# Performance work log

Hardware: AMD Instinct MI355X
Metric: run time of the kernel (lower is better)

The kernel has to match this reference:

```python
import jax, jax.numpy as jnp
import numpy as np

B, S, D, DFF, E, TOP_K = 4, 2048, 1024, 4096, 8, 2


def setup_inputs() -> dict:
    key = jax.random.key(0)
    ks = jax.random.split(key, 6)
    s = 0.02
    return {
        "x": jax.random.normal(ks[0], (B, S, D), dtype=jnp.float32),
        "gate_w": jax.random.normal(ks[1], (E, D), dtype=jnp.float32) * s,
        "w1": jax.random.normal(ks[2], (E, DFF, D), dtype=jnp.float32) * s,
        "b1": jax.random.normal(ks[3], (E, DFF), dtype=jnp.float32) * s,
        "w2": jax.random.normal(ks[4], (E, D, DFF), dtype=jnp.float32) * s,
        "b2": jax.random.normal(ks[5], (E, D), dtype=jnp.float32) * s,
    }


def _moe_forward(x, gate_w, w1, b1, w2, b2):
    b, s, d = x.shape
    xf = x.reshape(-1, d)                      # [T, D]
    T = xf.shape[0]
    e = gate_w.shape[0]
    logits = xf @ gate_w.T                     # [T, E]
    top_v, top_i = jax.lax.top_k(logits, TOP_K)  # [T, K]
    gw = jax.nn.softmax(top_v, axis=-1)          # [T, K]
    # load-balance loss (Switch Transformers): E * sum_i f_i * P_i
    probs = jax.nn.softmax(logits, axis=-1)
    f = jnp.mean(jax.nn.one_hot(jnp.argmax(logits, axis=-1), e, dtype=x.dtype), axis=0)
    lb_loss = e * jnp.sum(f * probs.mean(axis=0))
    # dense per-expert FFN (exact GELU, matching torch F.gelu default)
    h = jax.nn.gelu(jnp.einsum('td,efd->tef', xf, w1) + b1, approximate=False)  # [T,E,DFF]
    eo = jnp.einsum('tef,edf->ted', h, w2) + b2                                  # [T,E,D]
    # scatter top-k gate weights into dense [T, E] combine weights
    cw = jnp.zeros((T, e), dtype=x.dtype).at[jnp.arange(T)[:, None], top_i].add(gw)
    out = jnp.einsum('te,ted->td', cw, eo).reshape(b, s, d)
    return out, lb_loss


def reference(x, gate_w, w1, b1, w2, b2):
    return _moe_forward(x, gate_w, w1, b1, w2, b2)
```

## Files before the change

kernel.cpp:

```cpp
#include <hip/hip_runtime.h>
#include <cstdint>
#include <cstddef>

#define NEXP 8
#define NTOK 8192
#define DMODEL 1024
#define DFFN 4096
#define CAP 17408

typedef __bf16 bf16;
typedef bf16 bf16x8 __attribute__((ext_vector_type(8)));
typedef float f32x4 __attribute__((ext_vector_type(4)));

static constexpr size_t OFF_HDR  = 0;
static constexpr size_t OFF_CNTH = 4096;
static constexpr size_t OFF_AMH  = OFF_CNTH + 65536;
static constexpr size_t OFF_PSH  = OFF_AMH + 65536;
static constexpr size_t OFF_TOKE = OFF_PSH + 65536;
static constexpr size_t OFF_TOKG = OFF_TOKE + 65536;
static constexpr size_t OFF_TOKS = OFF_TOKG + 65536;
static constexpr size_t OFF_BB   = OFF_TOKS + 65536;
static constexpr size_t OFF_XG   = OFF_BB + 65536;
static constexpr size_t OFF_W1B  = OFF_XG  + (size_t)CAP * DMODEL * 2;
static constexpr size_t OFF_W2B  = OFF_W1B + (size_t)NEXP * DFFN * DMODEL * 2;
static constexpr size_t OFF_H    = OFF_W2B + (size_t)NEXP * DMODEL * DFFN * 2;
static constexpr size_t OFF_O    = OFF_H   + (size_t)CAP * DFFN * 2;


__global__ void k_zero16(uint4* __restrict__ p) {
    p[(size_t)blockIdx.x * 256 + threadIdx.x] = make_uint4(0u, 0u, 0u, 0u);
}

__global__ void k_cvt(const float* __restrict__ s, bf16* __restrict__ d, int n8) {
    int i = blockIdx.x * 256 + threadIdx.x;
    if (i >= n8) return;
    const float4* sp = (const float4*)s;
    float4 a = sp[2 * i], b = sp[2 * i + 1];
    bf16x8 pk;
    pk[0] = (bf16)a.x; pk[1] = (bf16)a.y; pk[2] = (bf16)a.z; pk[3] = (bf16)a.w;
    pk[4] = (bf16)b.x; pk[5] = (bf16)b.y; pk[6] = (bf16)b.z; pk[7] = (bf16)b.w;
    ((bf16x8*)d)[i] = pk;
}

__global__ void k_gate(const float* __restrict__ x, const float* __restrict__ gwt,
                       int* __restrict__ cnth, int* __restrict__ amh, float* __restrict__ psh,
                       int* __restrict__ toke, float* __restrict__ tokg) {
    int tid = threadIdx.x, w = tid >> 6, lane = tid & 63;
    int t = blockIdx.x * 4 + w;
    __shared__ int s_cnt[8]; __shared__ int s_am[8]; __shared__ float s_ps[8];
    if (tid < 8) { s_cnt[tid] = 0; s_am[tid] = 0; s_ps[tid] = 0.f; }
    __syncthreads();
    float acc[8] = {0.f,0.f,0.f,0.f,0.f,0.f,0.f,0.f};
    const float4* xr = (const float4*)(x + (size_t)t * DMODEL);
#pragma unroll
    for (int c = 0; c < 4; c++) {
        float4 xv = xr[c * 64 + lane];
#pragma unroll
        for (int e = 0; e < 8; e++) {
            float4 wv = ((const float4*)(gwt + e * DMODEL))[c * 64 + lane];
            acc[e] = fmaf(xv.x, wv.x, fmaf(xv.y, wv.y, fmaf(xv.z, wv.z, fmaf(xv.w, wv.w, acc[e]))));
        }
    }
#pragma unroll
    for (int o = 32; o; o >>= 1) {
#pragma unroll
        for (int e = 0; e < 8; e++) acc[e] += __shfl_xor(acc[e], o);
    }
    if (lane == 0) {
        int i0 = 0; float v0 = acc[0];
#pragma unroll
        for (int e = 1; e < 8; e++) if (acc[e] > v0) { v0 = acc[e]; i0 = e; }
        int i1 = -1; float v1 = -1e30f;
#pragma unroll
        for (int e = 0; e < 8; e++) if (e != i0 && acc[e] > v1) { v1 = acc[e]; i1 = e; }
        float ex = expf(v1 - v0);
        float g0 = 1.f / (1.f + ex);
        float g1 = ex / (1.f + ex);
        toke[2 * t] = i0; toke[2 * t + 1] = i1;
        tokg[2 * t] = g0; tokg[2 * t + 1] = g1;
        atomicAdd(&s_cnt[i0], 1); atomicAdd(&s_cnt[i1], 1); atomicAdd(&s_am[i0], 1);
        float p[8], sum = 0.f;
#pragma unroll
        for (int e = 0; e < 8; e++) { p[e] = expf(acc[e] - v0); sum += p[e]; }
        float inv = 1.f / sum;
#pragma unroll
        for (int e = 0; e < 8; e++) atomicAdd(&s_ps[e], p[e] * inv);
    }
    __syncthreads();
    if (tid < 8) {
        cnth[blockIdx.x * 8 + tid] = s_cnt[tid];
        amh[blockIdx.x * 8 + tid]  = s_am[tid];
        psh[blockIdx.x * 8 + tid]  = s_ps[tid];
    }
}

__global__ void k_offsets(const int* __restrict__ cnth, const int* __restrict__ amh,
                          const float* __restrict__ psh, int* __restrict__ hdr,
                          int* __restrict__ bb, float* __restrict__ lb_out) {
    __shared__ int sc[8][256];
    __shared__ int sa[8][256];
    __shared__ float sp[8][256];
    __shared__ int sOff[8];
    int tid = threadIdx.x;
    int tc[8] = {0,0,0,0,0,0,0,0}, la[8] = {0,0,0,0,0,0,0,0};
    float lp[8] = {0.f,0.f,0.f,0.f,0.f,0.f,0.f,0.f};
    for (int j = 0; j < 8; j++) {
        int b = tid * 8 + j;
#pragma unroll
        for (int e = 0; e < 8; e++) { tc[e] += cnth[b * 8 + e]; la[e] += amh[b * 8 + e]; lp[e] += psh[b * 8 + e]; }
    }
#pragma unroll
    for (int e = 0; e < 8; e++) { sc[e][tid] = tc[e]; sa[e][tid] = la[e]; sp[e][tid] = lp[e]; }
    __syncthreads();
    for (int s = 1; s < 256; s <<= 1) {
        int add[8];
#pragma unroll
        for (int e = 0; e < 8; e++) add[e] = (tid >= s) ? sc[e][tid - s] : 0;
        __syncthreads();
#pragma unroll
        for (int e = 0; e < 8; e++) sc[e][tid] += add[e];
        __syncthreads();
    }
    for (int s = 128; s > 0; s >>= 1) {
        if (tid < s) {
#pragma unroll
            for (int e = 0; e < 8; e++) { sa[e][tid] += sa[e][tid + s]; sp[e][tid] += sp[e][tid + s]; }
        }
        __syncthreads();
    }
    if (tid == 0) {
        int run = 0; float lb = 0.f;
        for (int e = 0; e < 8; e++) {
            int c = sc[e][255];
            hdr[e] = c;
            hdr[16 + e] = run;
            int pad = ((c + 127) >> 7) << 7;
            hdr[24 + e] = pad;
            sOff[e] = run;
            run += pad;
            lb += ((float)sa[e][0] / (float)NTOK) * (sp[e][0] / (float)NTOK);
        }
        lb_out[0] = 8.f * lb;
    }
    __syncthreads();
    int excl[8];
#pragma unroll
    for (int e = 0; e < 8; e++) excl[e] = sOff[e] + sc[e][tid] - tc[e];
    for (int j = 0; j < 8; j++) {
        int b = tid * 8 + j;
#pragma unroll
        for (int e = 0; e < 8; e++) {
            bb[b * 8 + e] = excl[e];
            excl[e] += cnth[b * 8 + e];
        }
    }
}

__global__ void k_scatter(const float* __restrict__ x, const int* __restrict__ bb,
                          const int* __restrict__ toke, int* __restrict__ toks,
                          bf16* __restrict__ Xg) {
    int tid = threadIdx.x, w = tid >> 6, lane = tid & 63;
    int t = blockIdx.x * 4 + w;
    int a_e = (lane < 8) ? toke[blockIdx.x * 8 + lane] : 0;
    int e0 = __shfl(a_e, 2 * w), e1 = __shfl(a_e, 2 * w + 1);
    int r0 = 0, r1 = 0;
    for (int j = 0; j < 2 * w; j++) {
        int ej = __shfl(a_e, j);
        r0 += (ej == e0);
        r1 += (ej == e1);
    }
    int s0 = bb[blockIdx.x * 8 + e0] + r0;
    int s1 = bb[blockIdx.x * 8 + e1] + r1;
    if (lane == 0) { toks[2 * t] = s0; toks[2 * t + 1] = s1; }
    const float4* xr = (const float4*)(x + (size_t)t * DMODEL);
    bf16* d0 = Xg + (size_t)s0 * DMODEL;
    bf16* d1 = Xg + (size_t)s1 * DMODEL;
#pragma unroll
    for (int c = 0; c < 2; c++) {
        int base = c * 512 + lane * 8;
        float4 u = xr[base >> 2], v = xr[(base >> 2) + 1];
        bf16x8 pk;
        pk[0] = (bf16)u.x; pk[1] = (bf16)u.y; pk[2] = (bf16)u.z; pk[3] = (bf16)u.w;
        pk[4] = (bf16)v.x; pk[5] = (bf16)v.y; pk[6] = (bf16)v.z; pk[7] = (bf16)v.w;
        *(bf16x8*)(d0 + base) = pk;
        *(bf16x8*)(d1 + base) = pk;
    }
}

__device__ __forceinline__ void gll16(const bf16* g, bf16* l) {
    __builtin_amdgcn_global_load_lds((const __attribute__((address_space(1))) unsigned int*)g,
                                     (__attribute__((address_space(3))) unsigned int*)l, 16, 0, 0);
}

__device__ __forceinline__ float gelu_fast(float x) {
    float x3 = x * x * x;
    float z = fmaf(0.0713548163f, x3, 1.5957691216f * x);
    float s = __builtin_amdgcn_rcpf(1.0f + __expf(-z));
    return x * s;
}

template <int KD, int ND, bool GELU_BF16>
__global__ __launch_bounds__(256) void k_gemm(
    const bf16* __restrict__ Abase, const bf16* __restrict__ Wbase,
    const float* __restrict__ bias, void* __restrict__ Cbase,
    const int* __restrict__ hdr) {
    int e = blockIdx.z;
    int padded = hdr[24 + e];
    int mt = blockIdx.y;
    if (mt * 128 >= padded) return;
    int row0 = hdr[16 + e] + mt * 128;
    int nt = blockIdx.x * 128;

    const bf16* A = Abase + (size_t)row0 * KD;
    const bf16* W = Wbase + (size_t)e * ND * KD + (size_t)nt * KD;

    __shared__ bf16 As[128 * 64];
    __shared__ bf16 Bs[128 * 64];

    int tid = threadIdx.x, w = tid >> 6, lane = tid & 63;
    int lrow = lane >> 3;
    int lcolswz = ((lane & 7) ^ lrow) * 8;
    int wm = (w & 1) * 64, wn = (w >> 1) * 64;
    int fr = lane & 15, quad = lane >> 4;
    int swz = quad ^ (fr & 7);

    f32x4 acc[4][4] = {};

    for (int k0 = 0; k0 < KD; k0 += 64) {
#pragma unroll
        for (int i = 0; i < 4; i++) {
            int rb = w * 32 + i * 8;
            gll16(A + (size_t)(rb + lrow) * KD + k0 + lcolswz, &As[rb * 64]);
            gll16(W + (size_t)(rb + lrow) * KD + k0 + lcolswz, &Bs[rb * 64]);
        }
        __syncthreads();
#pragma unroll
        for (int kk = 0; kk < 64; kk += 32) {
            int coff = (swz ^ (kk >> 3)) * 8;
            bf16x8 af[4], bfr[4];
#pragma unroll
            for (int i = 0; i < 4; i++) af[i]  = *(const bf16x8*)&As[(wm + i * 16 + fr) * 64 + coff];
#pragma unroll
            for (int j = 0; j < 4; j++) bfr[j] = *(const bf16x8*)&Bs[(wn + j * 16 + fr) * 64 + coff];
#pragma unroll
            for (int i = 0; i < 4; i++)
#pragma unroll
                for (int j = 0; j < 4; j++)
                    acc[i][j] = __builtin_amdgcn_mfma_f32_16x16x32_bf16(af[i], bfr[j], acc[i][j], 0, 0, 0);
        }
        __syncthreads();
    }

#pragma unroll
    for (int j = 0; j < 4; j++) {
        int col = nt + wn + j * 16 + fr;
        float bv = bias[e * ND + col];
#pragma unroll
        for (int i = 0; i < 4; i++) {
#pragma unroll
            for (int r = 0; r < 4; r++) {
                int row = row0 + wm + i * 16 + quad * 4 + r;
                float v = acc[i][j][r] + bv;
                if (GELU_BF16) {
                    v = gelu_fast(v);
                    ((bf16*)Cbase)[(size_t)row * ND + col] = (bf16)v;
                } else {
                    ((float*)Cbase)[(size_t)row * ND + col] = v;
                }
            }
        }
    }
}

__global__ void k_combine(const float* __restrict__ O, const int* __restrict__ toks,
                          const float* __restrict__ tokg, float* __restrict__ out) {
    int t = blockIdx.x;
    int s0 = toks[2 * t], s1 = toks[2 * t + 1];
    float g0 = tokg[2 * t], g1 = tokg[2 * t + 1];
    const float4* o0 = (const float4*)(O + (size_t)s0 * DMODEL);
    const float4* o1 = (const float4*)(O + (size_t)s1 * DMODEL);
    float4* dst = (float4*)(out + (size_t)t * DMODEL);
    int i = threadIdx.x;
    float4 a = o0[i], b = o1[i];
    float4 r;
    r.x = g0 * a.x + g1 * b.x;
    r.y = g0 * a.y + g1 * b.y;
    r.z = g0 * a.z + g1 * b.z;
    r.w = g0 * a.w + g1 * b.w;
    dst[i] = r;
}

extern "C" void kernel_launch(void* const* d_in, const int* in_sizes, int n_in,
                              void* d_out, int out_size, void* d_ws, size_t ws_size,
                              hipStream_t stream) {
    const float* x   = (const float*)d_in[0];
    const float* gwt = (const float*)d_in[1];
    const float* w1  = (const float*)d_in[2];
    const float* b1  = (const float*)d_in[3];
    const float* w2  = (const float*)d_in[4];
    const float* b2  = (const float*)d_in[5];
    float* out = (float*)d_out;

    char* ws = (char*)d_ws;
    int*   hdr  = (int*)(ws + OFF_HDR);
    int*   cnth = (int*)(ws + OFF_CNTH);
    int*   amh  = (int*)(ws + OFF_AMH);
    float* psh  = (float*)(ws + OFF_PSH);
    int*   toke = (int*)(ws + OFF_TOKE);
    float* tokg = (float*)(ws + OFF_TOKG);
    int*   toks = (int*)(ws + OFF_TOKS);
    int*   bb   = (int*)(ws + OFF_BB);
    bf16*  Xg   = (bf16*)(ws + OFF_XG);
    bf16*  w1b  = (bf16*)(ws + OFF_W1B);
    bf16*  w2b  = (bf16*)(ws + OFF_W2B);
    bf16*  H    = (bf16*)(ws + OFF_H);
    float* O    = (float*)(ws + OFF_O);

    k_zero16<<<8704, 256, 0, stream>>>((uint4*)(ws + OFF_XG));
    k_cvt<<<16384, 256, 0, stream>>>(w1, w1b, 4194304);
    k_cvt<<<16384, 256, 0, stream>>>(w2, w2b, 4194304);
    k_gate<<<2048, 256, 0, stream>>>(x, gwt, cnth, amh, psh, toke, tokg);
    k_offsets<<<1, 256, 0, stream>>>(cnth, amh, psh, hdr, bb, out + (size_t)NTOK * DMODEL);
    k_scatter<<<2048, 256, 0, stream>>>(x, bb, toke, toks, Xg);
    dim3 g1(DFFN / 128, 64, NEXP);
    k_gemm<DMODEL, DFFN, true><<<g1, 256, 0, stream>>>(Xg, w1b, b1, (void*)H, hdr);
    dim3 g2(DMODEL / 128, 64, NEXP);
    k_gemm<DFFN, DMODEL, false><<<g2, 256, 0, stream>>>(H, w2b, b2, (void*)O, hdr);
    k_combine<<<NTOK, 256, 0, stream>>>(O, toks, tokg, out);
}
```

Before: 899.4 us.

## Use 256x256 GEMM tiles with multi-buffered LDS pipeline and XCD-aware block swizzle

```diff
diff --git a/kernel.cpp b/kernel.cpp
--- a/kernel.cpp
+++ b/kernel.cpp
@@ -27,10 +27,6 @@
 static constexpr size_t OFF_O    = OFF_H   + (size_t)CAP * DFFN * 2;
 
 
-__global__ void k_zero16(uint4* __restrict__ p) {
-    p[(size_t)blockIdx.x * 256 + threadIdx.x] = make_uint4(0u, 0u, 0u, 0u);
-}
-
 __global__ void k_cvt(const float* __restrict__ s, bf16* __restrict__ d, int n8) {
     int i = blockIdx.x * 256 + threadIdx.x;
     if (i >= n8) return;
@@ -187,9 +183,24 @@
     }
 }
 
+__global__ void k_zeropad(const int* __restrict__ hdr, bf16* __restrict__ Xg) {
+    int e = blockIdx.x;
+    int cnt = hdr[e], off = hdr[16 + e], padded = hdr[24 + e];
+    int total = (padded - cnt) * (DMODEL / 8);
+    bf16x8* base = (bf16x8*)(Xg + (size_t)(off + cnt) * DMODEL);
+    bf16x8 z = {};
+    for (int i = threadIdx.x; i < total; i += 256) base[i] = z;
+}
+
 __device__ __forceinline__ void gll16(const bf16* g, bf16* l) {
     __builtin_amdgcn_global_load_lds((const __attribute__((address_space(1))) unsigned int*)g,
                                      (__attribute__((address_space(3))) unsigned int*)l, 16, 0, 0);
+}
+
+__device__ __forceinline__ void wg_bar() {
+    asm volatile("" ::: "memory");
+    __builtin_amdgcn_s_barrier();
+    asm volatile("" ::: "memory");
 }
 
 __device__ __forceinline__ float gelu_fast(float x) {
@@ -200,72 +211,115 @@
 }
 
 template <int KD, int ND, bool GELU_BF16>
-__global__ __launch_bounds__(256) void k_gemm(
+__global__ __launch_bounds__(512, 2) void k_gemm256(
     const bf16* __restrict__ Abase, const bf16* __restrict__ Wbase,
     const float* __restrict__ bias, void* __restrict__ Cbase,
     const int* __restrict__ hdr) {
-    int e = blockIdx.z;
+    constexpr int NT = KD / 32;
+    constexpr int GX = ND / 256;
+    constexpr int GYX = GX * 32;
+    extern __shared__ char smem[];
+
+    int flat = blockIdx.x + GX * (blockIdx.y + 32 * blockIdx.z);
+    constexpr int NPER = GYX * 8 / 8;
+    int swz = (flat & 7) * NPER + (flat >> 3);
+    int e   = swz / GYX;
+    int rem = swz - e * GYX;
+    int mt  = rem / GX;
+    int nt  = rem - mt * GX;
+
     int padded = hdr[24 + e];
-    int mt = blockIdx.y;
-    if (mt * 128 >= padded) return;
-    int row0 = hdr[16 + e] + mt * 128;
-    int nt = blockIdx.x * 128;
+    if (mt * 256 >= padded) return;
+    int mrem = padded - mt * 256; if (mrem > 256) mrem = 256;
+    int row0 = hdr[16 + e] + mt * 256;
 
     const bf16* A = Abase + (size_t)row0 * KD;
-    const bf16* W = Wbase + (size_t)e * ND * KD + (size_t)nt * KD;
-
-    __shared__ bf16 As[128 * 64];
-    __shared__ bf16 Bs[128 * 64];
-
-    int tid = threadIdx.x, w = tid >> 6, lane = tid & 63;
-    int lrow = lane >> 3;
-    int lcolswz = ((lane & 7) ^ lrow) * 8;
-    int wm = (w & 1) * 64, wn = (w >> 1) * 64;
+    const bf16* W = Wbase + (size_t)e * ND * KD + (size_t)(nt * 256) * KD;
+
+    int tid = threadIdx.x, wid = tid >> 6, lane = tid & 63;
+    int srow   = (wid << 4) + (lane >> 2);
+    int schunk = (lane & 3) ^ ((lane >> 2) & 3);
+    int wr = wid & 1, wc = wid >> 1;
+    int wm = wr << 7, wn = wc << 6;
     int fr = lane & 15, quad = lane >> 4;
-    int swz = quad ^ (fr & 7);
-
-    f32x4 acc[4][4] = {};
-
-    for (int k0 = 0; k0 < KD; k0 += 64) {
-#pragma unroll
-        for (int i = 0; i < 4; i++) {
-            int rb = w * 32 + i * 8;
-            gll16(A + (size_t)(rb + lrow) * KD + k0 + lcolswz, &As[rb * 64]);
-            gll16(W + (size_t)(rb + lrow) * KD + k0 + lcolswz, &Bs[rb * 64]);
-        }
-        __syncthreads();
-#pragma unroll
-        for (int kk = 0; kk < 64; kk += 32) {
-            int coff = (swz ^ (kk >> 3)) * 8;
-            bf16x8 af[4], bfr[4];
-#pragma unroll
-            for (int i = 0; i < 4; i++) af[i]  = *(const bf16x8*)&As[(wm + i * 16 + fr) * 64 + coff];
-#pragma unroll
-            for (int j = 0; j < 4; j++) bfr[j] = *(const bf16x8*)&Bs[(wn + j * 16 + fr) * 64 + coff];
-#pragma unroll
-            for (int i = 0; i < 4; i++)
-#pragma unroll
-                for (int j = 0; j < 4; j++)
-                    acc[i][j] = __builtin_amdgcn_mfma_f32_16x16x32_bf16(af[i], bfr[j], acc[i][j], 0, 0, 0);
-        }
-        __syncthreads();
+    int rchoff = (quad ^ (fr & 3)) << 4;
+
+    auto STAGE = [&](int u, int s) {
+        int b = u & 3;
+        int grow  = (s << 7) + srow;
+        int garow = (grow < mrem) ? grow : 0;
+        const bf16* ga = A + (size_t)garow * KD + u * 32 + (schunk << 3);
+        const bf16* gb = W + (size_t)grow  * KD + u * 32 + (schunk << 3);
+        bf16* la = (bf16*)(smem)         + (size_t)b * 8192 + (size_t)(((s << 7) + (wid << 4)) * 32);
+        bf16* lb = (bf16*)(smem + 65536) + (size_t)b * 8192 + (size_t)(((s << 7) + (wid << 4)) * 32);
+        gll16(ga, la);
+        gll16(gb, lb);
+    };
+    auto LDA = [&](int t, int i) -> bf16x8 {
+        const char* base = smem + (t & 3) * 16384;
+        return *(const bf16x8*)(base + ((wm + i * 16 + fr) << 6) + rchoff);
+    };
+    auto LDB = [&](int t, int j) -> bf16x8 {
+        const char* base = smem + 65536 + (t & 3) * 16384;
+        return *(const bf16x8*)(base + ((wn + j * 16 + fr) << 6) + rchoff);
+    };
+
+    STAGE(0, 0); STAGE(0, 1); STAGE(1, 0); STAGE(1, 1);
+    asm volatile("s_waitcnt vmcnt(4)" ::: "memory");
+    wg_bar();
+
+    f32x4 acc[8][4] = {};
+    bf16x8 a4[4], b4[4];
+
+#pragma unroll 1
+    for (int t = 0; t < NT; ++t) {
+#pragma unroll
+        for (int j = 0; j < 4; j++) b4[j] = LDB(t, j);
+#pragma unroll
+        for (int i = 0; i < 4; i++) a4[i] = LDA(t, i);
+        if (t + 2 < NT) STAGE(t + 2, 0);
+        wg_bar();
+        __builtin_amdgcn_s_setprio(1);
+#pragma unroll
+        for (int i = 0; i < 4; i++)
+#pragma unroll
+            for (int j = 0; j < 4; j++)
+                acc[i][j] = __builtin_amdgcn_mfma_f32_16x16x32_bf16(a4[i], b4[j], acc[i][j], 0, 0, 0);
+        __builtin_amdgcn_s_setprio(0);
+        wg_bar();
+#pragma unroll
+        for (int i = 0; i < 4; i++) a4[i] = LDA(t, i + 4);
+        if (t + 2 < NT) STAGE(t + 2, 1);
+        wg_bar();
+        __builtin_amdgcn_s_setprio(1);
+#pragma unroll
+        for (int i = 0; i < 4; i++)
+#pragma unroll
+            for (int j = 0; j < 4; j++)
+                acc[i + 4][j] = __builtin_amdgcn_mfma_f32_16x16x32_bf16(a4[i], b4[j], acc[i + 4][j], 0, 0, 0);
+        __builtin_amdgcn_s_setprio(0);
+        if (t < NT - 2)      { asm volatile("s_waitcnt vmcnt(4)" ::: "memory"); }
+        else if (t < NT - 1) { asm volatile("s_waitcnt vmcnt(0)" ::: "memory"); }
+        wg_bar();
     }
 
 #pragma unroll
     for (int j = 0; j < 4; j++) {
-        int col = nt + wn + j * 16 + fr;
+        int col = nt * 256 + wn + j * 16 + fr;
         float bv = bias[e * ND + col];
 #pragma unroll
-        for (int i = 0; i < 4; i++) {
+        for (int i = 0; i < 8; i++) {
 #pragma unroll
             for (int r = 0; r < 4; r++) {
-                int row = row0 + wm + i * 16 + quad * 4 + r;
-                float v = acc[i][j][r] + bv;
-                if (GELU_BF16) {
-                    v = gelu_fast(v);
-                    ((bf16*)Cbase)[(size_t)row * ND + col] = (bf16)v;
-                } else {
-                    ((float*)Cbase)[(size_t)row * ND + col] = v;
+                int rowt = wm + i * 16 + quad * 4 + r;
+                if (rowt < mrem) {
+                    float v = acc[i][j][r] + bv;
+                    size_t idx = (size_t)(row0 + rowt) * ND + col;
+                    if (GELU_BF16) {
+                        ((bf16*)Cbase)[idx] = (bf16)gelu_fast(v);
+                    } else {
+                        ((float*)Cbase)[idx] = v;
+                    }
                 }
             }
         }
@@ -316,15 +370,24 @@
     bf16*  H    = (bf16*)(ws + OFF_H);
     float* O    = (float*)(ws + OFF_O);
 
-    k_zero16<<<8704, 256, 0, stream>>>((uint4*)(ws + OFF_XG));
+    static bool s_attr = false;
+    if (!s_attr) {
+        (void)hipFuncSetAttribute(reinterpret_cast<const void*>(k_gemm256<DMODEL, DFFN, true>),
+                                  hipFuncAttributeMaxDynamicSharedMemorySize, 131072);
+        (void)hipFuncSetAttribute(reinterpret_cast<const void*>(k_gemm256<DFFN, DMODEL, false>),
+                                  hipFuncAttributeMaxDynamicSharedMemorySize, 131072);
+        s_attr = true;
+    }
+
     k_cvt<<<16384, 256, 0, stream>>>(w1, w1b, 4194304);
     k_cvt<<<16384, 256, 0, stream>>>(w2, w2b, 4194304);
     k_gate<<<2048, 256, 0, stream>>>(x, gwt, cnth, amh, psh, toke, tokg);
     k_offsets<<<1, 256, 0, stream>>>(cnth, amh, psh, hdr, bb, out + (size_t)NTOK * DMODEL);
+    k_zeropad<<<NEXP, 256, 0, stream>>>(hdr, Xg);
     k_scatter<<<2048, 256, 0, stream>>>(x, bb, toke, toks, Xg);
-    dim3 g1(DFFN / 128, 64, NEXP);
-    k_gemm<DMODEL, DFFN, true><<<g1, 256, 0, stream>>>(Xg, w1b, b1, (void*)H, hdr);
-    dim3 g2(DMODEL / 128, 64, NEXP);
-    k_gemm<DFFN, DMODEL, false><<<g2, 256, 0, stream>>>(H, w2b, b2, (void*)O, hdr);
+    dim3 g1(DFFN / 256, 32, NEXP);
+    k_gemm256<DMODEL, DFFN, true><<<g1, 512, 131072, stream>>>(Xg, w1b, b1, (void*)H, hdr);
+    dim3 g2(DMODEL / 256, 32, NEXP);
+    k_gemm256<DFFN, DMODEL, false><<<g2, 512, 131072, stream>>>(H, w2b, b2, (void*)O, hdr);
     k_combine<<<NTOK, 256, 0, stream>>>(O, toks, tokg, out);
 }
```

New measurement: 899.7 us. No clear change (+0.0%).
